# Kernel tuning notes

Hardware: AMD Instinct MI355X
Metric: run time of the kernel (lower is better)

Reference implementation:

```python
import jax, jax.numpy as jnp
import numpy as np

B, T, I, H, E, L = 128, 128, 512, 512, 256, 2


def _mk(key, shape, fan_in):
    return jax.random.uniform(key, shape, jnp.float32, -1.0, 1.0) / np.sqrt(fan_in)


def setup_inputs() -> dict:
    key = jax.random.key(0)
    ks = jax.random.split(key, 12)
    return {
        "x": jax.random.normal(ks[0], (B, T, I), jnp.float32),
        "extra_input": jax.random.normal(ks[1], (B, E), jnp.float32),
        # stacked per-layer weights, torch Linear convention: W is [out, in]
        "W_ir": _mk(ks[2], (L, H, I), I), "b_ir": _mk(ks[3], (L, H), I),
        "W_hr": _mk(ks[4], (L, H, H), H),
        "W_iz": _mk(ks[5], (L, H, I), I), "b_iz": _mk(ks[6], (L, H), I),
        "W_hz": _mk(ks[7], (L, H, H), H),
        "W_in": _mk(ks[8], (L, H, I), I), "b_in": _mk(ks[9], (L, H), I),
        "W_hn": _mk(ks[10], (L, H, H), H),
        "W_er": _mk(ks[11], (L, H, E), E),
    }


def reference(x, extra_input, W_ir, b_ir, W_hr, W_iz, b_iz, W_hz, W_in, b_in, W_hn, W_er):
    n_layers = W_ir.shape[0]
    # extra-input forget-gate contribution is constant over time: [L, B, H]
    er = jnp.einsum("be,lhe->lbh", extra_input, W_er)

    def cell(l, inp, h):
        r = jax.nn.sigmoid(inp @ W_ir[l].T + b_ir[l] + h @ W_hr[l].T + er[l])
        z = jax.nn.sigmoid(inp @ W_iz[l].T + b_iz[l] + h @ W_hz[l].T)
        n = jnp.tanh(inp @ W_in[l].T + b_in[l] + r * (h @ W_hn[l].T))
        return (1.0 - z) * n + z * h

    def step(hs, x_t):  # hs: [L, B, H], x_t: [B, I]
        inp = x_t
        new_hs = []
        for l in range(n_layers):
            h_new = cell(l, inp, hs[l])
            new_hs.append(h_new)
            inp = h_new
        return jnp.stack(new_hs, axis=0), inp  # emit last layer's hidden

    h0 = jnp.zeros((n_layers, x.shape[0], W_ir.shape[1]), x.dtype)
    h_final, outs = jax.lax.scan(step, h0, jnp.swapaxes(x, 0, 1))  # outs: [T, B, H]
    return jnp.swapaxes(outs, 0, 1), h_final
```

## Files before the change

### kernel.cpp

```cpp
#include <hip/hip_runtime.h>

typedef _Float16 f16;
typedef _Float16 f16x8 __attribute__((ext_vector_type(8)));
typedef float f32x4 __attribute__((ext_vector_type(4)));
typedef unsigned long long u64;
typedef unsigned u32;

#define BB 128
#define TT 128
#define IIN 512
#define HHID 512
#define EEX 256

__global__ void prep_kernel(const float* __restrict__ x,
    const float* __restrict__ W_ir, const float* __restrict__ W_iz, const float* __restrict__ W_in,
    const float* __restrict__ W_hr, const float* __restrict__ W_hz, const float* __restrict__ W_hn,
    f16* __restrict__ xb, f16* __restrict__ WiCat, f16* __restrict__ WhCat,
    u32* __restrict__ cnt)
{
  size_t idx = (size_t)blockIdx.x * 256 + threadIdx.x;

  const size_t NX = (size_t)TT * BB * (IIN / 8);
  const size_t NW = (size_t)2 * 1536 * (512 / 8);
  if (idx < NX) {
    int t = (int)(idx / (BB * 64));
    int rem = (int)(idx % (BB * 64));
    int b = rem >> 6;
    int k0 = (rem & 63) * 8;
    const float* src = x + ((size_t)b * TT + t) * IIN + k0;
    f16x8 v;
#pragma unroll
    for (int j = 0; j < 8; ++j) v[j] = (f16)src[j];
    *(f16x8*)(xb + ((size_t)t * BB + b) * IIN + k0) = v;
  } else if (idx < NX + 2 * NW) {
    size_t w = idx - NX;
    bool isI = w < NW;
    size_t w2 = isI ? w : w - NW;
    int l = (int)(w2 / (1536 * 64));
    int rem = (int)(w2 % (1536 * 64));
    int n = rem >> 6;
    int k0 = (rem & 63) * 8;
    int g = n >> 9, j = n & 511;
    const float* W = isI ? (g == 0 ? W_ir : (g == 1 ? W_iz : W_in))
                         : (g == 0 ? W_hr : (g == 1 ? W_hz : W_hn));
    const float* src = W + ((size_t)l * 512 + j) * 512 + k0;
    f16x8 v;
#pragma unroll
    for (int jj = 0; jj < 8; ++jj) v[jj] = (f16)src[jj];
    f16* dst = isI ? WiCat : WhCat;
    *(f16x8*)(dst + ((size_t)l * 1536 + n) * 512 + k0) = v;
  } else if (idx < NX + 2 * NW + 32768) {
    size_t z = idx - (NX + 2 * NW);
    __hip_atomic_store(cnt + z, 0u, __ATOMIC_RELAXED, __HIP_MEMORY_SCOPE_AGENT);
  }
}

__global__ void er_kernel(const float* __restrict__ extra, const float* __restrict__ W_er,
                          float* __restrict__ er)
{
  int idx = blockIdx.x * 256 + threadIdx.x;
  int l = idx >> 16;
  int b = (idx >> 9) & 127;
  int h = idx & 511;
  const float* e = extra + (size_t)b * EEX;
  const float* w = W_er + ((size_t)l * 512 + h) * EEX;
  float acc = 0.f;
#pragma unroll 4
  for (int k = 0; k < EEX; k += 4)
    acc += e[k] * w[k] + e[k + 1] * w[k + 1] + e[k + 2] * w[k + 2] + e[k + 3] * w[k + 3];
  er[idx] = acc;
}

__global__ __launch_bounds__(256, 1) void fused_recur(
    const f16* __restrict__ WiCat,
    const f16* __restrict__ WhCat,
    const f16* __restrict__ xb,
    const float* __restrict__ er,
    const float* __restrict__ b_ir, const float* __restrict__ b_iz, const float* __restrict__ b_in,
    float* __restrict__ outs,
    float* __restrict__ hfin,
    u32* __restrict__ h0x,
    u32* __restrict__ h1x,
    u32* __restrict__ cnt)
{
  const int tid = threadIdx.x;
  const int wave = tid >> 6, lane = tid & 63;
  const int bid = blockIdx.x;
  const int layer = bid >> 7;
  const int c = (bid >> 4) & 7;
  const int s = bid & 15;
  const int r16 = lane & 15, khi = lane >> 4;

  __shared__ f16 hL[16 * 520];
  __shared__ f16 xL[16 * 520];
  __shared__ float preH[6][16][17];
  __shared__ float preX[6][16][17];
  __shared__ float hf32[16 * 32];

  const bool isWi = wave >= 2;
  const int tb = (wave & 1) * 3;
  const f16* Wsrc = (isWi ? WiCat : WhCat) + (size_t)layer * 1536 * 512;
  f16x8 wf[3][16];
#pragma unroll
  for (int ti = 0; ti < 3; ++ti) {
    int gcl = (tb + ti) * 16 + r16;
    int g = gcl >> 5, cig = gcl & 31;
    const f16* wr = Wsrc + (size_t)(g * 512 + s * 32 + cig) * 512 + khi * 8;
#pragma unroll
    for (int cc = 0; cc < 16; ++cc) wf[ti][cc] = *(const f16x8*)(wr + cc * 32);
  }
#pragma unroll
  for (int ti = 0; ti < 3; ++ti)
#pragma unroll
    for (int cc = 0; cc < 16; ++cc)
      asm volatile("" : "+v"(wf[ti][cc]));

  {
    f16x8 z;
#pragma unroll
    for (int j = 0; j < 8; ++j) z[j] = (f16)0.f;
    for (int i = tid; i < 16 * 520 / 8; i += 256) ((f16x8*)hL)[i] = z;
    for (int i = tid; i < 512; i += 256) hf32[i] = 0.f;
  }

  const int row = tid >> 4, p = tid & 15;
  const int gr = c * 16 + row;
  const int j0 = 2 * p;
  float cbr[2], cbz[2], cbn[2];
#pragma unroll
  for (int e = 0; e < 2; ++e) {
    int jg = s * 32 + j0 + e;
    cbr[e] = b_ir[layer * 512 + jg] + er[((size_t)layer * 128 + gr) * 512 + jg];
    cbz[e] = b_iz[layer * 512 + jg];
    cbn[e] = b_in[layer * 512 + jg];
  }

  {
    u64 xr0[8];
    if (layer == 0) {
      const u64* sx = (const u64*)xb + ((size_t)0 * 128 + c * 16) * 128;
#pragma unroll
      for (int u = 0; u < 8; ++u) xr0[u] = sx[tid + u * 256];
    } else {
      if (tid == 0) {
        const u32* a = cnt + ((size_t)(0 * 8 + c) * 128 + 0) * 16;
        while (__hip_atomic_load(a, __ATOMIC_RELAXED, __HIP_MEMORY_SCOPE_AGENT) < 16u)
          __builtin_amdgcn_s_sleep(1);
      }
      __syncthreads();
      const u64* sx = (const u64*)h0x + ((size_t)0 * 128 + c * 16) * 128;
#pragma unroll
      for (int u = 0; u < 8; ++u)
        xr0[u] = __hip_atomic_load(sx + tid + u * 256, __ATOMIC_RELAXED, __HIP_MEMORY_SCOPE_AGENT);
    }
#pragma unroll
    for (int u = 0; u < 8; ++u) {
      int i = tid + u * 256, r = i >> 7, q = i & 127;
      *(u64*)(xL + r * 520 + q * 4) = xr0[u];
    }
  }
  __syncthreads();

  u32* hx_own = layer ? h1x : h0x;

  for (int t = 0; t < TT; ++t) {
    const f16* aL = isWi ? xL : hL;
    f32x4 ac0 = {0.f, 0.f, 0.f, 0.f}, ac1 = ac0, ac2 = ac0;
#pragma unroll
    for (int cc = 0; cc < 16; ++cc) {
      f16x8 a = *(const f16x8*)(aL + r16 * 520 + cc * 32 + khi * 8);
      ac0 = __builtin_amdgcn_mfma_f32_16x16x32_f16(a, wf[0][cc], ac0, 0, 0, 0);
      ac1 = __builtin_amdgcn_mfma_f32_16x16x32_f16(a, wf[1][cc], ac1, 0, 0, 0);
      ac2 = __builtin_amdgcn_mfma_f32_16x16x32_f16(a, wf[2][cc], ac2, 0, 0, 0);
    }
    {
      float (*pd)[16][17] = isWi ? preX : preH;
#pragma unroll
      for (int v = 0; v < 4; ++v) {
        pd[tb + 0][khi * 4 + v][r16] = ac0[v];
        pd[tb + 1][khi * 4 + v][r16] = ac1[v];
        pd[tb + 2][khi * 4 + v][r16] = ac2[v];
      }
    }
    __syncthreads();

    float hn[2];
#pragma unroll
    for (int e = 0; e < 2; ++e) {
      int j = j0 + e;
      int jz = 32 + j, jn = 64 + j;
      float sr = preX[j >> 4][row][j & 15] + cbr[e] + preH[j >> 4][row][j & 15];
      float sz = preX[jz >> 4][row][jz & 15] + cbz[e] + preH[jz >> 4][row][jz & 15];
      float pxn = preX[jn >> 4][row][jn & 15] + cbn[e];
      float phn = preH[jn >> 4][row][jn & 15];
      float rg = 1.f / (1.f + __expf(-sr));
      float zg = 1.f / (1.f + __expf(-sz));
      float xn = pxn + rg * phn;
      xn = fminf(15.f, fmaxf(-15.f, xn));
      float e2 = __expf(2.f * xn);
      float nn = (e2 - 1.f) / (e2 + 1.f);
      int li = row * 32 + j;
      float hold = hf32[li];
      float hv = (1.f - zg) * nn + zg * hold;
      hf32[li] = hv;
      hn[e] = hv;
    }
    {
      union { f16 h2[2]; u32 u; } pk;
      pk.h2[0] = (f16)hn[0]; pk.h2[1] = (f16)hn[1];
      __hip_atomic_store(hx_own + ((size_t)t * 128 + gr) * 256 + s * 16 + p, pk.u,
                         __ATOMIC_RELAXED, __HIP_MEMORY_SCOPE_AGENT);
    }
    if (layer == 1) {
      float* o = outs + ((size_t)gr * TT + t) * 512 + s * 32 + j0;
      o[0] = hn[0]; o[1] = hn[1];
    }
    if (t == TT - 1) {
      float* hf = hfin + ((size_t)layer * 128 + gr) * 512 + s * 32 + j0;
      hf[0] = hn[0]; hf[1] = hn[1];
      if (layer == 0) {
        asm volatile("s_waitcnt vmcnt(0)" ::: "memory");
        __syncthreads();
        if (tid == 0)
          __hip_atomic_fetch_add(cnt + ((size_t)(0 * 8 + c) * 128 + t) * 16, 1u,
                                 __ATOMIC_RELAXED, __HIP_MEMORY_SCOPE_AGENT);
      }
      break;
    }

    asm volatile("s_waitcnt vmcnt(0)" ::: "memory");
    __syncthreads();
    if (tid == 0)
      __hip_atomic_fetch_add(cnt + ((size_t)(layer * 8 + c) * 128 + t) * 16, 1u,
                             __ATOMIC_RELAXED, __HIP_MEMORY_SCOPE_AGENT);

    u64 xr[8];
    if (layer == 0) {
      const u64* sx = (const u64*)xb + ((size_t)(t + 1) * 128 + c * 16) * 128;
#pragma unroll
      for (int u = 0; u < 8; ++u) xr[u] = sx[tid + u * 256];
#pragma unroll
      for (int u = 0; u < 8; ++u) asm volatile("" : "+v"(xr[u]));
    }

    if (tid == 0) {
      const u32* a = cnt + ((size_t)(layer * 8 + c) * 128 + t) * 16;
      while (__hip_atomic_load(a, __ATOMIC_RELAXED, __HIP_MEMORY_SCOPE_AGENT) < 16u)
        __builtin_amdgcn_s_sleep(1);
      if (layer == 1) {
        const u32* b = cnt + ((size_t)(0 * 8 + c) * 128 + (t + 1)) * 16;
        while (__hip_atomic_load(b, __ATOMIC_RELAXED, __HIP_MEMORY_SCOPE_AGENT) < 16u)
          __builtin_amdgcn_s_sleep(1);
      }
    }
    __syncthreads();

    {
      const u64* hsrc = (const u64*)hx_own + ((size_t)t * 128 + c * 16) * 128;
      u64 hv[8];
#pragma unroll
      for (int u = 0; u < 8; ++u)
        hv[u] = __hip_atomic_load(hsrc + tid + u * 256, __ATOMIC_RELAXED, __HIP_MEMORY_SCOPE_AGENT);
      u64 xv[8];
      if (layer == 1) {
        const u64* xsrc = (const u64*)h0x + ((size_t)(t + 1) * 128 + c * 16) * 128;
#pragma unroll
        for (int u = 0; u < 8; ++u)
          xv[u] = __hip_atomic_load(xsrc + tid + u * 256, __ATOMIC_RELAXED, __HIP_MEMORY_SCOPE_AGENT);
      }
#pragma unroll
      for (int u = 0; u < 8; ++u) {
        int i = tid + u * 256, r = i >> 7, q = i & 127;
        *(u64*)(hL + r * 520 + q * 4) = hv[u];
      }
      if (layer == 0) {
#pragma unroll
        for (int u = 0; u < 8; ++u) {
          int i = tid + u * 256, r = i >> 7, q = i & 127;
          *(u64*)(xL + r * 520 + q * 4) = xr[u];
        }
      } else {
#pragma unroll
        for (int u = 0; u < 8; ++u) {
          int i = tid + u * 256, r = i >> 7, q = i & 127;
          *(u64*)(xL + r * 520 + q * 4) = xv[u];
        }
      }
    }
    __syncthreads();
  }
}

extern "C" void kernel_launch(void* const* d_in, const int* in_sizes, int n_in,
                              void* d_out, int out_size, void* d_ws, size_t ws_size,
                              hipStream_t stream) {
  const float* x     = (const float*)d_in[0];
  const float* extra = (const float*)d_in[1];
  const float* W_ir  = (const float*)d_in[2];
  const float* b_ir  = (const float*)d_in[3];
  const float* W_hr  = (const float*)d_in[4];
  const float* W_iz  = (const float*)d_in[5];
  const float* b_iz  = (const float*)d_in[6];
  const float* W_hz  = (const float*)d_in[7];
  const float* W_in  = (const float*)d_in[8];
  const float* b_in  = (const float*)d_in[9];
  const float* W_hn  = (const float*)d_in[10];
  const float* W_er  = (const float*)d_in[11];
  float* out = (float*)d_out;

  char* ws = (char*)d_ws;
  f16* WiCat = (f16*)(ws);
  f16* WhCat = (f16*)(ws + 3145728);
  f16* xb    = (f16*)(ws + 6291456);
  float* er  = (float*)(ws + 23068672);
  u32* h0x   = (u32*)(ws + 23592960);
  u32* h1x   = (u32*)(ws + 40370176);
  u32* cnt   = (u32*)(ws + 57147392);

  prep_kernel<<<5760, 256, 0, stream>>>(x, W_ir, W_iz, W_in, W_hr, W_hz, W_hn,
                                        xb, WiCat, WhCat, cnt);
  er_kernel<<<512, 256, 0, stream>>>(extra, W_er, er);

  float* outs = out;
  float* hfin = out + (size_t)BB * TT * HHID;

  fused_recur<<<256, 256, 0, stream>>>(WiCat, WhCat, xb, er, b_ir, b_iz, b_in,
                                       outs, hfin, h0x, h1x, cnt);
}
```

Before: 478.2 us.

## Replace block counters with per-wave tag flags polled by all lanes

Swaps the per-step atomic counter and thread-0 spin with __syncthreads for per-wave tag words. Each wave writes its own tag with the step value, and consumer waves poll all 64 producer tags in parallel, one lane per tag, which removes two block barriers and the atomic add from each step. The running hidden state also moves from shared memory into registers. The costs are a larger tag array to zero in the prep kernel and more global polling traffic. Memory ordering now relies on the vmcnt wait placed before each relaxed tag store.

```diff
diff --git a/kernel.cpp b/kernel.cpp
--- a/kernel.cpp
+++ b/kernel.cpp
@@ -12,11 +12,14 @@
 #define HHID 512
 #define EEX 256
 
+#define AL __ATOMIC_RELAXED
+#define SCA __HIP_MEMORY_SCOPE_AGENT
+
 __global__ void prep_kernel(const float* __restrict__ x,
     const float* __restrict__ W_ir, const float* __restrict__ W_iz, const float* __restrict__ W_in,
     const float* __restrict__ W_hr, const float* __restrict__ W_hz, const float* __restrict__ W_hn,
     f16* __restrict__ xb, f16* __restrict__ WiCat, f16* __restrict__ WhCat,
-    u32* __restrict__ cnt)
+    u32* __restrict__ tags)
 {
   size_t idx = (size_t)blockIdx.x * 256 + threadIdx.x;
 
@@ -49,9 +52,9 @@
     for (int jj = 0; jj < 8; ++jj) v[jj] = (f16)src[jj];
     f16* dst = isI ? WiCat : WhCat;
     *(f16x8*)(dst + ((size_t)l * 1536 + n) * 512 + k0) = v;
-  } else if (idx < NX + 2 * NW + 32768) {
+  } else if (idx < NX + 2 * NW + 131072) {
     size_t z = idx - (NX + 2 * NW);
-    __hip_atomic_store(cnt + z, 0u, __ATOMIC_RELAXED, __HIP_MEMORY_SCOPE_AGENT);
+    __hip_atomic_store(tags + z, 0u, AL, SCA);
   }
 }
 
@@ -79,9 +82,9 @@
     const float* __restrict__ b_ir, const float* __restrict__ b_iz, const float* __restrict__ b_in,
     float* __restrict__ outs,
     float* __restrict__ hfin,
-    u32* __restrict__ h0x,
-    u32* __restrict__ h1x,
-    u32* __restrict__ cnt)
+    u32* __restrict__ hx0,
+    u32* __restrict__ hx1,
+    u32* __restrict__ tags)
 {
   const int tid = threadIdx.x;
   const int wave = tid >> 6, lane = tid & 63;
@@ -95,7 +98,6 @@
   __shared__ f16 xL[16 * 520];
   __shared__ float preH[6][16][17];
   __shared__ float preX[6][16][17];
-  __shared__ float hf32[16 * 32];
 
   const bool isWi = wave >= 2;
   const int tb = (wave & 1) * 3;
@@ -120,7 +122,6 @@
 #pragma unroll
     for (int j = 0; j < 8; ++j) z[j] = (f16)0.f;
     for (int i = tid; i < 16 * 520 / 8; i += 256) ((f16x8*)hL)[i] = z;
-    for (int i = tid; i < 512; i += 256) hf32[i] = 0.f;
   }
 
   const int row = tid >> 4, p = tid & 15;
@@ -134,34 +135,37 @@
     cbz[e] = b_iz[layer * 512 + jg];
     cbn[e] = b_in[layer * 512 + jg];
   }
-
-  {
+  float hreg0 = 0.f, hreg1 = 0.f;
+
+  u32* hxOwn = layer ? hx1 : hx0;
+  u32* tagOwn = tags + (size_t)layer * TT * 8 * 64;
+  const u32* tag0 = tags;
+
+  if (layer == 0) {
+    const u64* sx = (const u64*)xb + ((size_t)0 * 128 + c * 16) * 128;
     u64 xr0[8];
-    if (layer == 0) {
-      const u64* sx = (const u64*)xb + ((size_t)0 * 128 + c * 16) * 128;
-#pragma unroll
-      for (int u = 0; u < 8; ++u) xr0[u] = sx[tid + u * 256];
-    } else {
-      if (tid == 0) {
-        const u32* a = cnt + ((size_t)(0 * 8 + c) * 128 + 0) * 16;
-        while (__hip_atomic_load(a, __ATOMIC_RELAXED, __HIP_MEMORY_SCOPE_AGENT) < 16u)
-          __builtin_amdgcn_s_sleep(1);
-      }
-      __syncthreads();
-      const u64* sx = (const u64*)h0x + ((size_t)0 * 128 + c * 16) * 128;
-#pragma unroll
-      for (int u = 0; u < 8; ++u)
-        xr0[u] = __hip_atomic_load(sx + tid + u * 256, __ATOMIC_RELAXED, __HIP_MEMORY_SCOPE_AGENT);
-    }
+#pragma unroll
+    for (int u = 0; u < 8; ++u) xr0[u] = sx[tid + 256 * u];
 #pragma unroll
     for (int u = 0; u < 8; ++u) {
-      int i = tid + u * 256, r = i >> 7, q = i & 127;
+      int i = tid + 256 * u, r = i >> 7, q = i & 127;
       *(u64*)(xL + r * 520 + q * 4) = xr0[u];
     }
+  } else {
+    const u32* tp = tag0 + ((size_t)0 * 8 + c) * 64 + lane;
+    while (__hip_atomic_load(tp, AL, SCA) != 1u) {}
+    const u64* sx = (const u64*)hx0 + ((size_t)0 * 128 + c * 16) * 128;
+    u64 xv0[8];
+#pragma unroll
+    for (int u = 0; u < 8; ++u)
+      xv0[u] = __hip_atomic_load(sx + tid + 256 * u, AL, SCA);
+#pragma unroll
+    for (int u = 0; u < 8; ++u) {
+      int i = tid + 256 * u, r = i >> 7, q = i & 127;
+      *(u64*)(xL + r * 520 + q * 4) = xv0[u];
+    }
   }
   __syncthreads();
-
-  u32* hx_own = layer ? h1x : h0x;
 
   for (int t = 0; t < TT; ++t) {
     const f16* aL = isWi ? xL : hL;
@@ -199,17 +203,15 @@
       xn = fminf(15.f, fmaxf(-15.f, xn));
       float e2 = __expf(2.f * xn);
       float nn = (e2 - 1.f) / (e2 + 1.f);
-      int li = row * 32 + j;
-      float hold = hf32[li];
+      float hold = e ? hreg1 : hreg0;
       float hv = (1.f - zg) * nn + zg * hold;
-      hf32[li] = hv;
+      if (e) hreg1 = hv; else hreg0 = hv;
       hn[e] = hv;
     }
     {
       union { f16 h2[2]; u32 u; } pk;
       pk.h2[0] = (f16)hn[0]; pk.h2[1] = (f16)hn[1];
-      __hip_atomic_store(hx_own + ((size_t)t * 128 + gr) * 256 + s * 16 + p, pk.u,
-                         __ATOMIC_RELAXED, __HIP_MEMORY_SCOPE_AGENT);
+      __hip_atomic_store(hxOwn + ((size_t)t * 128 + gr) * 256 + s * 16 + p, pk.u, AL, SCA);
     }
     if (layer == 1) {
       float* o = outs + ((size_t)gr * TT + t) * 512 + s * 32 + j0;
@@ -218,73 +220,67 @@
     if (t == TT - 1) {
       float* hf = hfin + ((size_t)layer * 128 + gr) * 512 + s * 32 + j0;
       hf[0] = hn[0]; hf[1] = hn[1];
-      if (layer == 0) {
-        asm volatile("s_waitcnt vmcnt(0)" ::: "memory");
-        __syncthreads();
-        if (tid == 0)
-          __hip_atomic_fetch_add(cnt + ((size_t)(0 * 8 + c) * 128 + t) * 16, 1u,
-                                 __ATOMIC_RELAXED, __HIP_MEMORY_SCOPE_AGENT);
-      }
-      break;
-    }
-
-    asm volatile("s_waitcnt vmcnt(0)" ::: "memory");
-    __syncthreads();
-    if (tid == 0)
-      __hip_atomic_fetch_add(cnt + ((size_t)(layer * 8 + c) * 128 + t) * 16, 1u,
-                             __ATOMIC_RELAXED, __HIP_MEMORY_SCOPE_AGENT);
+    }
+
+    if (layer == 0 || t < TT - 1) {
+      asm volatile("s_waitcnt vmcnt(0)" ::: "memory");
+      if (lane == 0)
+        __hip_atomic_store(tagOwn + ((size_t)t * 8 + c) * 64 + s * 4 + wave,
+                           (u32)(t + 1), AL, SCA);
+    }
+    if (t == TT - 1) break;
 
     u64 xr[8];
     if (layer == 0) {
       const u64* sx = (const u64*)xb + ((size_t)(t + 1) * 128 + c * 16) * 128;
 #pragma unroll
-      for (int u = 0; u < 8; ++u) xr[u] = sx[tid + u * 256];
-#pragma unroll
-      for (int u = 0; u < 8; ++u) asm volatile("" : "+v"(xr[u]));
-    }
-
-    if (tid == 0) {
-      const u32* a = cnt + ((size_t)(layer * 8 + c) * 128 + t) * 16;
-      while (__hip_atomic_load(a, __ATOMIC_RELAXED, __HIP_MEMORY_SCOPE_AGENT) < 16u)
-        __builtin_amdgcn_s_sleep(1);
-      if (layer == 1) {
-        const u32* b = cnt + ((size_t)(0 * 8 + c) * 128 + (t + 1)) * 16;
-        while (__hip_atomic_load(b, __ATOMIC_RELAXED, __HIP_MEMORY_SCOPE_AGENT) < 16u)
-          __builtin_amdgcn_s_sleep(1);
+      for (int u = 0; u < 8; ++u) xr[u] = sx[tid + 256 * u];
+    }
+
+    {
+      const u32* tpa = tagOwn + ((size_t)t * 8 + c) * 64 + lane;
+      const u32 wa = (u32)(t + 1);
+      bool da = false;
+      bool db = (layer == 0);
+      const u32* tpb = tag0 + ((size_t)(t + 1) * 8 + c) * 64 + lane;
+      const u32 wb = (u32)(t + 2);
+      while (!(da && db)) {
+        if (!da) da = (__hip_atomic_load(tpa, AL, SCA) == wa);
+        if (!db) db = (__hip_atomic_load(tpb, AL, SCA) == wb);
       }
     }
-    __syncthreads();
-
+
+    u64 hv8[8];
     {
-      const u64* hsrc = (const u64*)hx_own + ((size_t)t * 128 + c * 16) * 128;
-      u64 hv[8];
+      const u64* hs = (const u64*)hxOwn + ((size_t)t * 128 + c * 16) * 128;
 #pragma unroll
       for (int u = 0; u < 8; ++u)
-        hv[u] = __hip_atomic_load(hsrc + tid + u * 256, __ATOMIC_RELAXED, __HIP_MEMORY_SCOPE_AGENT);
-      u64 xv[8];
-      if (layer == 1) {
-        const u64* xsrc = (const u64*)h0x + ((size_t)(t + 1) * 128 + c * 16) * 128;
-#pragma unroll
-        for (int u = 0; u < 8; ++u)
-          xv[u] = __hip_atomic_load(xsrc + tid + u * 256, __ATOMIC_RELAXED, __HIP_MEMORY_SCOPE_AGENT);
+        hv8[u] = __hip_atomic_load(hs + tid + 256 * u, AL, SCA);
+    }
+    u64 xv8[8];
+    if (layer == 1) {
+      const u64* xs = (const u64*)hx0 + ((size_t)(t + 1) * 128 + c * 16) * 128;
+#pragma unroll
+      for (int u = 0; u < 8; ++u)
+        xv8[u] = __hip_atomic_load(xs + tid + 256 * u, AL, SCA);
+    }
+
+#pragma unroll
+    for (int u = 0; u < 8; ++u) {
+      int i = tid + 256 * u, r = i >> 7, q = i & 127;
+      *(u64*)(hL + r * 520 + q * 4) = hv8[u];
+    }
+    if (layer == 0) {
+#pragma unroll
+      for (int u = 0; u < 8; ++u) {
+        int i = tid + 256 * u, r = i >> 7, q = i & 127;
+        *(u64*)(xL + r * 520 + q * 4) = xr[u];
       }
+    } else {
 #pragma unroll
       for (int u = 0; u < 8; ++u) {
-        int i = tid + u * 256, r = i >> 7, q = i & 127;
-        *(u64*)(hL + r * 520 + q * 4) = hv[u];
-      }
-      if (layer == 0) {
-#pragma unroll
-        for (int u = 0; u < 8; ++u) {
-          int i = tid + u * 256, r = i >> 7, q = i & 127;
-          *(u64*)(xL + r * 520 + q * 4) = xr[u];
-        }
-      } else {
-#pragma unroll
-        for (int u = 0; u < 8; ++u) {
-          int i = tid + u * 256, r = i >> 7, q = i & 127;
-          *(u64*)(xL + r * 520 + q * 4) = xv[u];
-        }
+        int i = tid + 256 * u, r = i >> 7, q = i & 127;
+        *(u64*)(xL + r * 520 + q * 4) = xv8[u];
       }
     }
     __syncthreads();
@@ -313,17 +309,17 @@
   f16* WhCat = (f16*)(ws + 3145728);
   f16* xb    = (f16*)(ws + 6291456);
   float* er  = (float*)(ws + 23068672);
-  u32* h0x   = (u32*)(ws + 23592960);
-  u32* h1x   = (u32*)(ws + 40370176);
-  u32* cnt   = (u32*)(ws + 57147392);
-
-  prep_kernel<<<5760, 256, 0, stream>>>(x, W_ir, W_iz, W_in, W_hr, W_hz, W_hn,
-                                        xb, WiCat, WhCat, cnt);
+  u32* hx0   = (u32*)(ws + 23592960);
+  u32* hx1   = (u32*)(ws + 40370176);
+  u32* tags  = (u32*)(ws + 57147392);
+
+  prep_kernel<<<6144, 256, 0, stream>>>(x, W_ir, W_iz, W_in, W_hr, W_hz, W_hn,
+                                        xb, WiCat, WhCat, tags);
   er_kernel<<<512, 256, 0, stream>>>(extra, W_er, er);
 
   float* outs = out;
   float* hfin = out + (size_t)BB * TT * HHID;
 
   fused_recur<<<256, 256, 0, stream>>>(WiCat, WhCat, xb, er, b_ir, b_iz, b_in,
-                                       outs, hfin, h0x, h1x, cnt);
+                                       outs, hfin, hx0, hx1, tags);
 }
```

Result: slower. 579.8 us (+21.2%).
